# Performance work log

Measured on AMD Instinct MI355X. Metric: run time of the kernel, lower is better.

Reference implementation:

```python
import jax, jax.numpy as jnp
import numpy as np

B, S, D, H = 4, 2048, 512, 8
HD = D // H


def _xavier(key, shape):
    fan_in, fan_out = shape[1], shape[0]
    limit = float(np.sqrt(6.0 / (fan_in + fan_out)))
    return jax.random.uniform(key, shape, jnp.float32, -limit, limit)


def setup_inputs() -> dict:
    key = jax.random.key(0)
    ks = jax.random.split(key, 7)
    return {
        "query": jax.random.normal(ks[0], (B, S, D), jnp.float32),
        "key": jax.random.normal(ks[1], (B, S, D), jnp.float32),
        "value": jax.random.normal(ks[2], (B, S, D), jnp.float32),
        "Wq": _xavier(ks[3], (D, D)), "bq": jnp.zeros((D,), jnp.float32),
        "Wk": _xavier(ks[4], (D, D)), "bk": jnp.zeros((D,), jnp.float32),
        "Wv": _xavier(ks[5], (D, D)), "bv": jnp.zeros((D,), jnp.float32),
        "Wo": _xavier(ks[6], (D, D)), "bo": jnp.zeros((D,), jnp.float32),
    }


def _split_heads(x):
    # [B,S,D] -> [B,H,S,HD]
    return x.reshape(B, S, H, HD).transpose(0, 2, 1, 3)


def reference(query, key, value, Wq, bq, Wk, bk, Wv, bv, Wo, bo):
    # torch Linear: y = x @ W.T + b
    Q = _split_heads(query @ Wq.T + bq)
    K = _split_heads(key @ Wk.T + bk)
    V = _split_heads(value @ Wv.T + bv)
    scale = 1.0 / jnp.sqrt(jnp.asarray(HD, Q.dtype))
    logits = jnp.einsum("bhqd,bhkd->bhqk", Q, K) * scale  # [B,H,S,S]
    attn = jax.nn.softmax(logits, axis=-1)
    ctx = jnp.einsum("bhqk,bhkd->bhqd", attn, V)
    ctx = ctx.transpose(0, 2, 1, 3).reshape(B, S, D)
    return ctx @ Wo.T + bo
```

## Files before the change

### kernel.cpp

```cpp
#include <hip/hip_runtime.h>
#include <hip/hip_bf16.h>


#define BB 4
#define SS 2048
#define DD 512
#define HH 8
#define HDD 64

typedef __bf16 bf16;
typedef __bf16 bf16x8 __attribute__((ext_vector_type(8)));
typedef float f32x4 __attribute__((ext_vector_type(4)));
typedef float f32x16 __attribute__((ext_vector_type(16)));

__device__ __forceinline__ int swz(int row, int byteInRow) {
    return row * 128 + (byteInRow ^ ((row & 7) << 4));
}

__device__ __forceinline__ void gload16(const void* g, void* l) {
    __builtin_amdgcn_global_load_lds(
        (const __attribute__((address_space(1))) void*)g,
        (__attribute__((address_space(3))) void*)l, 16, 0, 0);
}

__global__ __launch_bounds__(256) void cvt_bf16(
    const float* __restrict__ xq, const float* __restrict__ xk, const float* __restrict__ xv,
    const float* __restrict__ wq, const float* __restrict__ wk, const float* __restrict__ wv,
    const float* __restrict__ wo,
    bf16* __restrict__ xqb, bf16* __restrict__ xkb, bf16* __restrict__ xvb,
    bf16* __restrict__ wqb, bf16* __restrict__ wkb, bf16* __restrict__ wvb,
    bf16* __restrict__ wob)
{
    const int NX = BB * SS * DD / 4;
    const int NW = DD * DD / 4;
    const int total = 3 * NX + 4 * NW;
    for (int g = blockIdx.x * 256 + threadIdx.x; g < total; g += gridDim.x * 256) {
        const float* src; bf16* dst; int off;
        if (g < 3 * NX) {
            int s = g >> 20; off = g & (NX - 1);
            src = s == 0 ? xq : s == 1 ? xk : xv;
            dst = s == 0 ? xqb : s == 1 ? xkb : xvb;
        } else {
            int gg = g - 3 * NX; int s = gg >> 16; off = gg & (NW - 1);
            src = s == 0 ? wq : s == 1 ? wk : s == 2 ? wv : wo;
            dst = s == 0 ? wqb : s == 1 ? wkb : s == 2 ? wvb : wob;
        }
        float4 v = ((const float4*)src)[off];
        union { bf16 h[4]; ushort4 u; } c;
        c.h[0] = (bf16)v.x; c.h[1] = (bf16)v.y; c.h[2] = (bf16)v.z; c.h[3] = (bf16)v.w;
        ((ushort4*)dst)[off] = c.u;
    }
}

__global__ __launch_bounds__(256) void gemm_qkv(
    const bf16* __restrict__ Xq, const bf16* __restrict__ Xk, const bf16* __restrict__ Xv,
    const bf16* __restrict__ Wq, const bf16* __restrict__ Wk, const bf16* __restrict__ Wv,
    const float* __restrict__ bq, const float* __restrict__ bk, const float* __restrict__ bv,
    bf16* __restrict__ Qb, bf16* __restrict__ Kb, bf16* __restrict__ Vt)
{
    const int lin = blockIdx.x;
    const int w = (lin & 7) * 96 + (lin >> 3);
    const int z = w >> 8, rem = w & 255;
    const int m0 = (rem >> 2) * 128, n0 = (rem & 3) * 128;

    const bf16* __restrict__ A  = (z == 0) ? Xq : (z == 1) ? Xk : Xv;
    const bf16* __restrict__ Wt = (z == 0) ? Wq : (z == 1) ? Wk : Wv;
    const float* __restrict__ bias = (z == 0) ? bq : (z == 1) ? bk : bv;

    __shared__ char lds[32768];
    char* As = lds;
    char* Bs = lds + 16384;

    const int t = threadIdx.x, wid = t >> 6, lane = t & 63;
    const int wr = wid >> 1, wc = wid & 1;
    const int lr = lane & 15, lg = lane >> 4;

    float bv4[4];
#pragma unroll
    for (int ni = 0; ni < 4; ni++) bv4[ni] = bias[n0 + wc * 64 + ni * 16 + lr];

    const int srow = lane >> 3, s_l = (lane & 7) ^ srow;

    f32x4 acc[4][4] = {};

    for (int k0 = 0; k0 < DD; k0 += 64) {
#pragma unroll
        for (int i = 0; i < 4; i++) {
            int row = 32 * wid + 8 * i + srow;
            gload16(A  + (size_t)(m0 + row) * DD + k0 + s_l * 8, As + (32 * wid + 8 * i) * 128);
            gload16(Wt + (size_t)(n0 + row) * DD + k0 + s_l * 8, Bs + (32 * wid + 8 * i) * 128);
        }
        __syncthreads();
#pragma unroll
        for (int kk = 0; kk < 2; kk++) {
            bf16x8 af[4], bfr[4];
#pragma unroll
            for (int mi = 0; mi < 4; mi++)
                af[mi] = *(const bf16x8*)(As + swz(wr * 64 + mi * 16 + lr, kk * 64 + lg * 16));
#pragma unroll
            for (int ni = 0; ni < 4; ni++)
                bfr[ni] = *(const bf16x8*)(Bs + swz(wc * 64 + ni * 16 + lr, kk * 64 + lg * 16));
#pragma unroll
            for (int mi = 0; mi < 4; mi++)
#pragma unroll
                for (int ni = 0; ni < 4; ni++)
                    acc[mi][ni] = __builtin_amdgcn_mfma_f32_16x16x32_bf16(af[mi], bfr[ni], acc[mi][ni], 0, 0, 0);
        }
        __syncthreads();
    }

#pragma unroll
    for (int mi = 0; mi < 4; mi++)
#pragma unroll
        for (int ni = 0; ni < 4; ni++) {
            int col = n0 + wc * 64 + ni * 16 + lr;
#pragma unroll
            for (int j = 0; j < 4; j++) {
                int row = m0 + wr * 64 + mi * 16 + lg * 4 + j;
                float v = acc[mi][ni][j] + bv4[ni];
                if (z == 0) {
                    Qb[(size_t)row * DD + col] = (bf16)v;
                } else if (z == 1) {
                    Kb[(size_t)row * DD + col] = (bf16)v;
                } else {
                    int b = row >> 11, s = row & 2047, h = col >> 6, d = col & 63;
                    Vt[((((size_t)b * HH + h) * HDD + d) << 11) + s] = (bf16)v;
                }
            }
        }
}

__global__ __launch_bounds__(512) void attn_kernel(
    const bf16* __restrict__ Qb, const bf16* __restrict__ Kb,
    const bf16* __restrict__ Vt, bf16* __restrict__ Ctx)
{
    __shared__ char lds[65536];
    const int t = threadIdx.x, wid = t >> 6, lane = t & 63;
    const int grp = wid >> 2, qw = wid & 3;
    const int l31 = lane & 31, hi = lane >> 5;
    const int lin = blockIdx.x;
    const int wk = (lin & 7) * 64 + (lin >> 3);
    const int qt = wk & 15, bh = wk >> 4;
    const int b = bh >> 3, h = bh & 7;
    const int q0 = qt * 128 + qw * 32;

    const bf16* Qp = Qb + ((size_t)b * SS + q0) * DD + h * HDD;
    const bf16* Kp = Kb + (size_t)b * SS * DD + h * HDD;
    const bf16* Vp = Vt + ((size_t)b * HH + h) * HDD * SS;

    const float qscale = 0.125f * 1.4426950408889634f;
    bf16x8 qf[4];
#pragma unroll
    for (int dk = 0; dk < 4; dk++) {
        bf16x8 v = *(const bf16x8*)(Qp + (size_t)l31 * DD + dk * 16 + hi * 8);
#pragma unroll
        for (int e = 0; e < 8; e++) v[e] = (bf16)((float)v[e] * qscale);
        qf[dk] = v;
    }

    bf16x8 ones;
#pragma unroll
    for (int e = 0; e < 8; e++) ones[e] = (bf16)1.0f;

    const int srow = lane >> 3, s_l = (lane & 7) ^ srow;
    const size_t koff = (size_t)(16 * qw + srow) * DD + s_l * 8;
    const size_t voff = (size_t)(16 * qw + srow) * SS + s_l * 8;

#define STAGE(buf, kvb) do {                                                   \
        char* Kd = lds + grp * 16384 + (buf) * 8192 + qw * 2048;               \
        char* Vd = lds + 32768 + grp * 16384 + (buf) * 8192 + qw * 2048;       \
        gload16(Kp + koff + (size_t)(kvb) * DD, Kd);                           \
        gload16(Kp + koff + 8 * DD + (size_t)(kvb) * DD, Kd + 1024);           \
        gload16(Vp + voff + (kvb), Vd);                                        \
        gload16(Vp + voff + 8 * SS + (kvb), Vd + 1024);                        \
    } while (0)

    STAGE(0, grp * 64);

    f32x16 ctx0 = {}, ctx1 = {}, l4 = {};
    __syncthreads();

    const int NI = SS / 128;
    for (int it = 0; it < NI; ++it) {
        const int cur = it & 1;
        const char* Ks = lds + grp * 16384 + cur * 8192;
        const char* Vs = lds + 32768 + grp * 16384 + cur * 8192;
        if (it + 1 < NI) STAGE(cur ^ 1, (it + 1) * 128 + grp * 64);

        f32x16 p0 = {}, p1 = {};
        __builtin_amdgcn_s_setprio(1);
#pragma unroll
        for (int dk = 0; dk < 4; dk++) {
            bf16x8 kf0 = *(const bf16x8*)(Ks + swz(l31,      dk * 32 + hi * 16));
            bf16x8 kf1 = *(const bf16x8*)(Ks + swz(32 + l31, dk * 32 + hi * 16));
            p0 = __builtin_amdgcn_mfma_f32_32x32x16_bf16(kf0, qf[dk], p0, 0, 0, 0);
            p1 = __builtin_amdgcn_mfma_f32_32x32x16_bf16(kf1, qf[dk], p1, 0, 0, 0);
        }
        __builtin_amdgcn_s_setprio(0);

#pragma unroll
        for (int r = 0; r < 16; r++) {
            p0[r] = __builtin_amdgcn_exp2f(p0[r]);
            p1[r] = __builtin_amdgcn_exp2f(p1[r]);
        }

#define PVBLOCK(P, NTOFF) do {                                                       \
        union { bf16 h[8]; bf16x8 v; } F0, F1;                                       \
        _Pragma("unroll")                                                            \
        for (int e = 0; e < 8; e++) { F0.h[e] = (bf16)P[e]; F1.h[e] = (bf16)P[8 + e]; } \
        l4 = __builtin_amdgcn_mfma_f32_32x32x16_bf16(F0.v, ones, l4, 0, 0, 0);       \
        l4 = __builtin_amdgcn_mfma_f32_32x32x16_bf16(F1.v, ones, l4, 0, 0, 0);       \
        union { ushort4 q[2]; bf16x8 v; } v00, v01, v10, v11;                        \
        v00.q[0] = *(const ushort4*)(Vs + swz(l31,      (NTOFF) + 8 * hi));          \
        v00.q[1] = *(const ushort4*)(Vs + swz(l31,      (NTOFF) + 16 + 8 * hi));     \
        v01.q[0] = *(const ushort4*)(Vs + swz(32 + l31, (NTOFF) + 8 * hi));          \
        v01.q[1] = *(const ushort4*)(Vs + swz(32 + l31, (NTOFF) + 16 + 8 * hi));     \
        v10.q[0] = *(const ushort4*)(Vs + swz(l31,      (NTOFF) + 32 + 8 * hi));     \
        v10.q[1] = *(const ushort4*)(Vs + swz(l31,      (NTOFF) + 48 + 8 * hi));     \
        v11.q[0] = *(const ushort4*)(Vs + swz(32 + l31, (NTOFF) + 32 + 8 * hi));     \
        v11.q[1] = *(const ushort4*)(Vs + swz(32 + l31, (NTOFF) + 48 + 8 * hi));     \
        ctx0 = __builtin_amdgcn_mfma_f32_32x32x16_bf16(F0.v, v00.v, ctx0, 0, 0, 0);  \
        ctx0 = __builtin_amdgcn_mfma_f32_32x32x16_bf16(F1.v, v10.v, ctx0, 0, 0, 0);  \
        ctx1 = __builtin_amdgcn_mfma_f32_32x32x16_bf16(F0.v, v01.v, ctx1, 0, 0, 0);  \
        ctx1 = __builtin_amdgcn_mfma_f32_32x32x16_bf16(F1.v, v11.v, ctx1, 0, 0, 0);  \
    } while (0)

        PVBLOCK(p0, 0);
        PVBLOCK(p1, 64);
#undef PVBLOCK
        __syncthreads();
    }
#undef STAGE

    if (grp == 1) {
        float* dst = (float*)(lds + qw * 12288);
#pragma unroll
        for (int r = 0; r < 16; r++) {
            dst[r * 64 + lane]        = ctx0[r];
            dst[(16 + r) * 64 + lane] = ctx1[r];
            dst[(32 + r) * 64 + lane] = l4[r];
        }
    }
    __syncthreads();
    if (grp == 0) {
        const float* src = (const float*)(lds + qw * 12288);
#pragma unroll
        for (int r = 0; r < 16; r++) {
            ctx0[r] += src[r * 64 + lane];
            ctx1[r] += src[(16 + r) * 64 + lane];
            l4[r]   += src[(32 + r) * 64 + lane];
        }
#pragma unroll
        for (int r = 0; r < 16; r++) {
            int q = (r & 3) + 8 * (r >> 2) + 4 * hi;
            float inv = 1.0f / l4[r];
            size_t base = ((size_t)b * SS + q0 + q) * DD + h * HDD;
            Ctx[base + l31]      = (bf16)(ctx0[r] * inv);
            Ctx[base + 32 + l31] = (bf16)(ctx1[r] * inv);
        }
    }
}

__global__ __launch_bounds__(256) void gemm_out(
    const bf16* __restrict__ A, const bf16* __restrict__ Wt,
    const float* __restrict__ bias, float* __restrict__ Out)
{
    const int lin = blockIdx.x;
    const int w = (lin & 7) * 32 + (lin >> 3);
    const int m0 = (w >> 2) * 128, n0 = (w & 3) * 128;

    __shared__ char lds[32768];
    char* As = lds;
    char* Bs = lds + 16384;

    const int t = threadIdx.x, wid = t >> 6, lane = t & 63;
    const int wr = wid >> 1, wc = wid & 1;
    const int lr = lane & 15, lg = lane >> 4;

    float bv4[4];
#pragma unroll
    for (int ni = 0; ni < 4; ni++) bv4[ni] = bias[n0 + wc * 64 + ni * 16 + lr];

    const int srow = lane >> 3, s_l = (lane & 7) ^ srow;

    f32x4 acc[4][4] = {};

    for (int k0 = 0; k0 < DD; k0 += 64) {
#pragma unroll
        for (int i = 0; i < 4; i++) {
            int row = 32 * wid + 8 * i + srow;
            gload16(A  + (size_t)(m0 + row) * DD + k0 + s_l * 8, As + (32 * wid + 8 * i) * 128);
            gload16(Wt + (size_t)(n0 + row) * DD + k0 + s_l * 8, Bs + (32 * wid + 8 * i) * 128);
        }
        __syncthreads();
#pragma unroll
        for (int kk = 0; kk < 2; kk++) {
            bf16x8 af[4], bfr[4];
#pragma unroll
            for (int mi = 0; mi < 4; mi++)
                af[mi] = *(const bf16x8*)(As + swz(wr * 64 + mi * 16 + lr, kk * 64 + lg * 16));
#pragma unroll
            for (int ni = 0; ni < 4; ni++)
                bfr[ni] = *(const bf16x8*)(Bs + swz(wc * 64 + ni * 16 + lr, kk * 64 + lg * 16));
#pragma unroll
            for (int mi = 0; mi < 4; mi++)
#pragma unroll
                for (int ni = 0; ni < 4; ni++)
                    acc[mi][ni] = __builtin_amdgcn_mfma_f32_16x16x32_bf16(af[mi], bfr[ni], acc[mi][ni], 0, 0, 0);
        }
        __syncthreads();
    }

#pragma unroll
    for (int mi = 0; mi < 4; mi++)
#pragma unroll
        for (int ni = 0; ni < 4; ni++) {
            int col = n0 + wc * 64 + ni * 16 + lr;
#pragma unroll
            for (int j = 0; j < 4; j++) {
                int row = m0 + wr * 64 + mi * 16 + lg * 4 + j;
                Out[(size_t)row * DD + col] = acc[mi][ni][j] + bv4[ni];
            }
        }
}

extern "C" void kernel_launch(void* const* d_in, const int* in_sizes, int n_in,
                              void* d_out, int out_size, void* d_ws, size_t ws_size,
                              hipStream_t stream) {
    (void)in_sizes; (void)n_in; (void)out_size; (void)ws_size;
    const float* q  = (const float*)d_in[0];
    const float* k  = (const float*)d_in[1];
    const float* v  = (const float*)d_in[2];
    const float* Wq = (const float*)d_in[3]; const float* bq = (const float*)d_in[4];
    const float* Wk = (const float*)d_in[5]; const float* bk = (const float*)d_in[6];
    const float* Wv = (const float*)d_in[7]; const float* bv = (const float*)d_in[8];
    const float* Wo = (const float*)d_in[9]; const float* bo = (const float*)d_in[10];
    float* out = (float*)d_out;

    char* ws = (char*)d_ws;
    const size_t MD2 = (size_t)BB * SS * DD * 2;
    const size_t WB  = (size_t)DD * DD * 2;
    bf16* Qb  = (bf16*)(ws);
    bf16* Kb  = (bf16*)(ws + MD2);
    bf16* Vt  = (bf16*)(ws + 2 * MD2);
    bf16* Ctx = (bf16*)(ws + 3 * MD2);
    bf16* Xqb = Ctx;
    bf16* Xkb = (bf16*)(ws + 4 * MD2);
    bf16* Xvb = (bf16*)(ws + 5 * MD2);
    bf16* Wqb = (bf16*)(ws + 6 * MD2);
    bf16* Wkb = (bf16*)(ws + 6 * MD2 + WB);
    bf16* Wvb = (bf16*)(ws + 6 * MD2 + 2 * WB);
    bf16* Wob = (bf16*)(ws + 6 * MD2 + 3 * WB);

    cvt_bf16<<<2048, 256, 0, stream>>>(q, k, v, Wq, Wk, Wv, Wo,
                                       Xqb, Xkb, Xvb, Wqb, Wkb, Wvb, Wob);

    gemm_qkv<<<768, 256, 0, stream>>>(Xqb, Xkb, Xvb, Wqb, Wkb, Wvb,
                                      bq, bk, bv, Qb, Kb, Vt);

    attn_kernel<<<512, 512, 0, stream>>>(Qb, Kb, Vt, Ctx);

    gemm_out<<<256, 256, 0, stream>>>(Ctx, Wob, bo, out);
}
```

Baseline: 121.4 us.

## Halve GEMM N-tile to 64 to double block count, raise PV MFMA priority

Both projection GEMMs move from 128x128 to 128x64 output tiles, with each warp owning 32 rows by 64 columns. This doubles the grid (gemm_out goes from 256 to 512 blocks on a 256-CU part) so more CUs have work, and it cuts LDS use per block. The cost is less operand reuse per block and more total loads of the A tile. Separately, the attention kernel raises wave priority around the PV MFMA block.

```diff
diff --git a/kernel.cpp b/kernel.cpp
--- a/kernel.cpp
+++ b/kernel.cpp
@@ -59,49 +59,52 @@
     bf16* __restrict__ Qb, bf16* __restrict__ Kb, bf16* __restrict__ Vt)
 {
     const int lin = blockIdx.x;
-    const int w = (lin & 7) * 96 + (lin >> 3);
-    const int z = w >> 8, rem = w & 255;
-    const int m0 = (rem >> 2) * 128, n0 = (rem & 3) * 128;
+    const int w = (lin & 7) * 192 + (lin >> 3);
+    const int z = w / 512, rem = w & 511;
+    const int m0 = (rem >> 3) * 128, n0 = (rem & 7) * 64;
 
     const bf16* __restrict__ A  = (z == 0) ? Xq : (z == 1) ? Xk : Xv;
     const bf16* __restrict__ Wt = (z == 0) ? Wq : (z == 1) ? Wk : Wv;
     const float* __restrict__ bias = (z == 0) ? bq : (z == 1) ? bk : bv;
 
-    __shared__ char lds[32768];
+    __shared__ char lds[24576];
     char* As = lds;
     char* Bs = lds + 16384;
 
     const int t = threadIdx.x, wid = t >> 6, lane = t & 63;
-    const int wr = wid >> 1, wc = wid & 1;
     const int lr = lane & 15, lg = lane >> 4;
 
     float bv4[4];
 #pragma unroll
-    for (int ni = 0; ni < 4; ni++) bv4[ni] = bias[n0 + wc * 64 + ni * 16 + lr];
+    for (int ni = 0; ni < 4; ni++) bv4[ni] = bias[n0 + ni * 16 + lr];
 
     const int srow = lane >> 3, s_l = (lane & 7) ^ srow;
 
-    f32x4 acc[4][4] = {};
+    f32x4 acc[2][4] = {};
 
     for (int k0 = 0; k0 < DD; k0 += 64) {
 #pragma unroll
         for (int i = 0; i < 4; i++) {
             int row = 32 * wid + 8 * i + srow;
-            gload16(A  + (size_t)(m0 + row) * DD + k0 + s_l * 8, As + (32 * wid + 8 * i) * 128);
-            gload16(Wt + (size_t)(n0 + row) * DD + k0 + s_l * 8, Bs + (32 * wid + 8 * i) * 128);
+            gload16(A + (size_t)(m0 + row) * DD + k0 + s_l * 8, As + (32 * wid + 8 * i) * 128);
+        }
+#pragma unroll
+        for (int i = 0; i < 2; i++) {
+            int row = 16 * wid + 8 * i + srow;
+            gload16(Wt + (size_t)(n0 + row) * DD + k0 + s_l * 8, Bs + (16 * wid + 8 * i) * 128);
         }
         __syncthreads();
 #pragma unroll
         for (int kk = 0; kk < 2; kk++) {
-            bf16x8 af[4], bfr[4];
-#pragma unroll
-            for (int mi = 0; mi < 4; mi++)
-                af[mi] = *(const bf16x8*)(As + swz(wr * 64 + mi * 16 + lr, kk * 64 + lg * 16));
+            bf16x8 af[2], bfr[4];
+#pragma unroll
+            for (int mi = 0; mi < 2; mi++)
+                af[mi] = *(const bf16x8*)(As + swz(wid * 32 + mi * 16 + lr, kk * 64 + lg * 16));
 #pragma unroll
             for (int ni = 0; ni < 4; ni++)
-                bfr[ni] = *(const bf16x8*)(Bs + swz(wc * 64 + ni * 16 + lr, kk * 64 + lg * 16));
-#pragma unroll
-            for (int mi = 0; mi < 4; mi++)
+                bfr[ni] = *(const bf16x8*)(Bs + swz(ni * 16 + lr, kk * 64 + lg * 16));
+#pragma unroll
+            for (int mi = 0; mi < 2; mi++)
 #pragma unroll
                 for (int ni = 0; ni < 4; ni++)
                     acc[mi][ni] = __builtin_amdgcn_mfma_f32_16x16x32_bf16(af[mi], bfr[ni], acc[mi][ni], 0, 0, 0);
@@ -110,13 +113,13 @@
     }
 
 #pragma unroll
-    for (int mi = 0; mi < 4; mi++)
+    for (int mi = 0; mi < 2; mi++)
 #pragma unroll
         for (int ni = 0; ni < 4; ni++) {
-            int col = n0 + wc * 64 + ni * 16 + lr;
+            int col = n0 + ni * 16 + lr;
 #pragma unroll
             for (int j = 0; j < 4; j++) {
-                int row = m0 + wr * 64 + mi * 16 + lg * 4 + j;
+                int row = m0 + wid * 32 + mi * 16 + lg * 4 + j;
                 float v = acc[mi][ni][j] + bv4[ni];
                 if (z == 0) {
                     Qb[(size_t)row * DD + col] = (bf16)v;
@@ -204,6 +207,7 @@
             p1[r] = __builtin_amdgcn_exp2f(p1[r]);
         }
 
+        __builtin_amdgcn_s_setprio(1);
 #define PVBLOCK(P, NTOFF) do {                                                       \
         union { bf16 h[8]; bf16x8 v; } F0, F1;                                       \
         _Pragma("unroll")                                                            \
@@ -228,6 +232,7 @@
         PVBLOCK(p0, 0);
         PVBLOCK(p1, 64);
 #undef PVBLOCK
+        __builtin_amdgcn_s_setprio(0);
         __syncthreads();
     }
 #undef STAGE
@@ -266,44 +271,47 @@
     const float* __restrict__ bias, float* __restrict__ Out)
 {
     const int lin = blockIdx.x;
-    const int w = (lin & 7) * 32 + (lin >> 3);
-    const int m0 = (w >> 2) * 128, n0 = (w & 3) * 128;
-
-    __shared__ char lds[32768];
+    const int w = (lin & 7) * 64 + (lin >> 3);
+    const int m0 = (w >> 3) * 128, n0 = (w & 7) * 64;
+
+    __shared__ char lds[24576];
     char* As = lds;
     char* Bs = lds + 16384;
 
     const int t = threadIdx.x, wid = t >> 6, lane = t & 63;
-    const int wr = wid >> 1, wc = wid & 1;
     const int lr = lane & 15, lg = lane >> 4;
 
     float bv4[4];
 #pragma unroll
-    for (int ni = 0; ni < 4; ni++) bv4[ni] = bias[n0 + wc * 64 + ni * 16 + lr];
+    for (int ni = 0; ni < 4; ni++) bv4[ni] = bias[n0 + ni * 16 + lr];
 
     const int srow = lane >> 3, s_l = (lane & 7) ^ srow;
 
-    f32x4 acc[4][4] = {};
+    f32x4 acc[2][4] = {};
 
     for (int k0 = 0; k0 < DD; k0 += 64) {
 #pragma unroll
         for (int i = 0; i < 4; i++) {
             int row = 32 * wid + 8 * i + srow;
-            gload16(A  + (size_t)(m0 + row) * DD + k0 + s_l * 8, As + (32 * wid + 8 * i) * 128);
-            gload16(Wt + (size_t)(n0 + row) * DD + k0 + s_l * 8, Bs + (32 * wid + 8 * i) * 128);
+            gload16(A + (size_t)(m0 + row) * DD + k0 + s_l * 8, As + (32 * wid + 8 * i) * 128);
+        }
+#pragma unroll
+        for (int i = 0; i < 2; i++) {
+            int row = 16 * wid + 8 * i + srow;
+            gload16(Wt + (size_t)(n0 + row) * DD + k0 + s_l * 8, Bs + (16 * wid + 8 * i) * 128);
         }
         __syncthreads();
 #pragma unroll
         for (int kk = 0; kk < 2; kk++) {
-            bf16x8 af[4], bfr[4];
-#pragma unroll
-            for (int mi = 0; mi < 4; mi++)
-                af[mi] = *(const bf16x8*)(As + swz(wr * 64 + mi * 16 + lr, kk * 64 + lg * 16));
+            bf16x8 af[2], bfr[4];
+#pragma unroll
+            for (int mi = 0; mi < 2; mi++)
+                af[mi] = *(const bf16x8*)(As + swz(wid * 32 + mi * 16 + lr, kk * 64 + lg * 16));
 #pragma unroll
             for (int ni = 0; ni < 4; ni++)
-                bfr[ni] = *(const bf16x8*)(Bs + swz(wc * 64 + ni * 16 + lr, kk * 64 + lg * 16));
-#pragma unroll
-            for (int mi = 0; mi < 4; mi++)
+                bfr[ni] = *(const bf16x8*)(Bs + swz(ni * 16 + lr, kk * 64 + lg * 16));
+#pragma unroll
+            for (int mi = 0; mi < 2; mi++)
 #pragma unroll
                 for (int ni = 0; ni < 4; ni++)
                     acc[mi][ni] = __builtin_amdgcn_mfma_f32_16x16x32_bf16(af[mi], bfr[ni], acc[mi][ni], 0, 0, 0);
@@ -312,13 +320,13 @@
     }
 
 #pragma unroll
-    for (int mi = 0; mi < 4; mi++)
+    for (int mi = 0; mi < 2; mi++)
 #pragma unroll
         for (int ni = 0; ni < 4; ni++) {
-            int col = n0 + wc * 64 + ni * 16 + lr;
+            int col = n0 + ni * 16 + lr;
 #pragma unroll
             for (int j = 0; j < 4; j++) {
-                int row = m0 + wr * 64 + mi * 16 + lg * 4 + j;
+                int row = m0 + wid * 32 + mi * 16 + lg * 4 + j;
                 Out[(size_t)row * DD + col] = acc[mi][ni][j] + bv4[ni];
             }
         }
@@ -355,10 +363,10 @@
     cvt_bf16<<<2048, 256, 0, stream>>>(q, k, v, Wq, Wk, Wv, Wo,
                                        Xqb, Xkb, Xvb, Wqb, Wkb, Wvb, Wob);
 
-    gemm_qkv<<<768, 256, 0, stream>>>(Xqb, Xkb, Xvb, Wqb, Wkb, Wvb,
-                                      bq, bk, bv, Qb, Kb, Vt);
+    gemm_qkv<<<1536, 256, 0, stream>>>(Xqb, Xkb, Xvb, Wqb, Wkb, Wvb,
+                                       bq, bk, bv, Qb, Kb, Vt);
 
     attn_kernel<<<512, 512, 0, stream>>>(Qb, Kb, Vt, Ctx);
 
-    gemm_out<<<256, 256, 0, stream>>>(Ctx, Wob, bo, out);
-}
+    gemm_out<<<512, 256, 0, stream>>>(Ctx, Wob, bo, out);
+}
```

Result: no change. 121.8 us (+0.4%).
